# Optimization experiments

Measured on AMD Instinct MI355X. Metric: run time of the kernel, lower is better.

Reference implementation:

```python
import jax, jax.numpy as jnp
import numpy as np

HEADS = 16


def setup_inputs() -> dict:
    key = jax.random.key(0)
    k1, k2, k3, k4 = jax.random.split(key, 4)
    B, S, D = 2, 2048, 1024
    x = jax.random.normal(k1, (B, S, D), dtype=jnp.float32)
    scale = 0.02
    Wq = jax.random.normal(k2, (D, D), dtype=jnp.float32) * scale
    Wk = jax.random.normal(k3, (D, D), dtype=jnp.float32) * scale
    Wv = jax.random.normal(k4, (D, D), dtype=jnp.float32) * scale
    return {"x": x, "Wq": Wq, "Wk": Wk, "Wv": Wv}


def reference(x, Wq, Wk, Wv):
    B, S, D = x.shape
    H = HEADS
    dh = D // H
    # project and split heads: (B, S, D) -> (B, H, S, dh)
    def split_heads(t):
        return t.reshape(B, S, H, dh).transpose(0, 2, 1, 3)

    q = split_heads(x @ Wq)
    k = split_heads(x @ Wk)
    v = split_heads(x @ Wv)

    # scores: (B, H, S, S)
    scores = jnp.einsum("bhqd,bhkd->bhqk", q, k)
    causal_mask = jnp.triu(jnp.ones((S, S), dtype=bool), k=1)  # True above diagonal -> masked
    scores = jnp.where(causal_mask, -jnp.inf, scores) / jnp.sqrt(jnp.float32(dh))
    weights = jax.nn.softmax(scores, axis=-1)
    # dropout is identity at inference (eval mode)
    ctx = jnp.einsum("bhqk,bhkd->bhqd", weights, v)  # (B, H, S, dh)
    return ctx.transpose(0, 2, 1, 3).reshape(B, S, D)
```

## Files before the change

### kernel.cpp

```cpp
#include <hip/hip_runtime.h>
#include <hip/hip_bf16.h>
#include <cstdint>

#define BATCH  2
#define SEQ    2048
#define DMODEL 1024
#define NH     16
#define DH     64

typedef short bf16x8 __attribute__((ext_vector_type(8)));
typedef float f32x4  __attribute__((ext_vector_type(4)));
typedef unsigned short u16;

#define MFMA16(a, b, c) __builtin_amdgcn_mfma_f32_16x16x32_bf16((a), (b), (c), 0, 0, 0)

#define GLL(gp, lp) __builtin_amdgcn_global_load_lds( \
    (const __attribute__((address_space(1))) void*)(gp), \
    (__attribute__((address_space(3))) void*)(lp), 16, 0, 0)

#define SCL 0.18033688011112042f

#if __has_builtin(__builtin_amdgcn_exp2f)
#define EXP2(x) __builtin_amdgcn_exp2f(x)
#else
#define EXP2(x) __expf((x) * 0.69314718055994531f)
#endif

static __device__ __forceinline__ u16 f2bf(float f) {
  union { float f; unsigned int i; } u; u.f = f;
  unsigned int r = u.i + 0x7FFFu + ((u.i >> 16) & 1u);
  return (u16)(r >> 16);
}

__global__ __launch_bounds__(256) void convert_x_kernel(const float* __restrict__ X,
                                                        u16* __restrict__ Xb) {
  int idx = (blockIdx.x * 256 + threadIdx.x) * 8;
  float4 a = *reinterpret_cast<const float4*>(X + idx);
  float4 b = *reinterpret_cast<const float4*>(X + idx + 4);
  union { bf16x8 v; u16 u[8]; } pk;
  pk.u[0]=f2bf(a.x); pk.u[1]=f2bf(a.y); pk.u[2]=f2bf(a.z); pk.u[3]=f2bf(a.w);
  pk.u[4]=f2bf(b.x); pk.u[5]=f2bf(b.y); pk.u[6]=f2bf(b.z); pk.u[7]=f2bf(b.w);
  *reinterpret_cast<bf16x8*>(Xb + idx) = pk.v;
}

__global__ __launch_bounds__(256) void transpose_w_kernel(const float* __restrict__ W0,
                                                          const float* __restrict__ W1,
                                                          const float* __restrict__ W2,
                                                          u16* __restrict__ Wt) {
  const float* W = (blockIdx.z == 0) ? W0 : (blockIdx.z == 1) ? W1 : W2;
  const float sc = (blockIdx.z == 0) ? SCL : 1.0f;
  u16* out = Wt + (size_t)blockIdx.z * DMODEL * DMODEL;
  __shared__ float T[32][33];
  const int t = threadIdx.x;
  const int k0 = blockIdx.x * 32, n0 = blockIdx.y * 32;
  {
    int r = t >> 3, c = (t & 7) * 4;
    float4 v = *reinterpret_cast<const float4*>(W + (size_t)(k0 + r) * DMODEL + n0 + c);
    T[r][c] = v.x; T[r][c+1] = v.y; T[r][c+2] = v.z; T[r][c+3] = v.w;
  }
  __syncthreads();
  {
    int n = t >> 3, k = (t & 7) * 4;
    union { unsigned long long ll; u16 u[4]; } pk;
    pk.u[0] = f2bf(T[k][n] * sc);   pk.u[1] = f2bf(T[k+1][n] * sc);
    pk.u[2] = f2bf(T[k+2][n] * sc); pk.u[3] = f2bf(T[k+3][n] * sc);
    *reinterpret_cast<unsigned long long*>(out + (size_t)(n0 + n) * DMODEL + k0 + k) = pk.ll;
  }
}

__global__ __launch_bounds__(256) void qkv_mfma_kernel(const u16* __restrict__ Xb,
                                                       const u16* __restrict__ Wt,
                                                       u16* __restrict__ Y) {
  __shared__ u16 As[128 * 64];
  __shared__ u16 Bs[128 * 64];
  char* Ab = (char*)As; char* Bb = (char*)Bs;
  const int t = threadIdx.x;
  const int lane = t & 63;
  const int w = t >> 6;
  const int wr = w >> 1, wc = w & 1;
  const int l15 = lane & 15, lg = lane >> 4;
  const int row0 = blockIdx.x * 128;
  const int col0 = blockIdx.y * 128;
  const int z = blockIdx.z;
  const u16* Wz = Wt + (size_t)z * DMODEL * DMODEL;
  u16* Yz = Y + (size_t)z * ((size_t)BATCH * SEQ * DMODEL);

  f32x4 acc[4][4];
  #pragma unroll
  for (int mt = 0; mt < 4; ++mt)
    #pragma unroll
    for (int nt = 0; nt < 4; ++nt)
      acc[mt][nt] = (f32x4){0.f, 0.f, 0.f, 0.f};

  size_t aofs[4], bofs[4];
  #pragma unroll
  for (int it = 0; it < 4; ++it) {
    int row = it * 32 + (t >> 3);
    int sl  = (t & 7) ^ (row & 7);
    aofs[it] = (size_t)(row0 + row) * DMODEL + sl * 8;
    bofs[it] = (size_t)(col0 + row) * DMODEL + sl * 8;
  }

  for (int k0 = 0; k0 < DMODEL; k0 += 64) {
    __syncthreads();
    #pragma unroll
    for (int it = 0; it < 4; ++it) {
      GLL(Xb + aofs[it] + k0, Ab + it * 4096 + w * 1024);
      GLL(Wz + bofs[it] + k0, Bb + it * 4096 + w * 1024);
    }
    __syncthreads();
    #pragma unroll
    for (int c = 0; c < 2; ++c) {
      bf16x8 am[4], bn[4];
      int kof = c * 64 + lg * 16;
      #pragma unroll
      for (int mt = 0; mt < 4; ++mt) {
        int row = wr * 64 + mt * 16 + l15;
        am[mt] = *reinterpret_cast<const bf16x8*>(Ab + row * 128 + (kof ^ ((row & 7) << 4)));
      }
      #pragma unroll
      for (int nt = 0; nt < 4; ++nt) {
        int row = wc * 64 + nt * 16 + l15;
        bn[nt] = *reinterpret_cast<const bf16x8*>(Bb + row * 128 + (kof ^ ((row & 7) << 4)));
      }
      #pragma unroll
      for (int mt = 0; mt < 4; ++mt)
        #pragma unroll
        for (int nt = 0; nt < 4; ++nt)
          acc[mt][nt] = MFMA16(am[mt], bn[nt], acc[mt][nt]);
    }
  }

  #pragma unroll
  for (int mt = 0; mt < 4; ++mt) {
    #pragma unroll
    for (int i = 0; i < 4; ++i) {
      int bs = row0 + wr * 64 + mt * 16 + lg * 4 + i;
      int b = bs >> 11, s = bs & (SEQ - 1);
      #pragma unroll
      for (int nt = 0; nt < 4; ++nt) {
        int d = col0 + wc * 64 + nt * 16 + l15;
        int h = d >> 6, dd = d & (DH - 1);
        size_t off = (((size_t)b * NH + h) * SEQ + s) * DH + dd;
        Yz[off] = f2bf(acc[mt][nt][i]);
      }
    }
  }
}

__global__ __launch_bounds__(256) void transpose_v_kernel(const u16* __restrict__ V,
                                                          u16* __restrict__ Vt) {
  __shared__ u16 L[64][72];
  const int sb = blockIdx.x, h = blockIdx.y, b = blockIdx.z;
  const size_t hin  = ((size_t)b * NH + h) * (size_t)SEQ * DH;
  const size_t hout = ((size_t)b * NH + h) * (size_t)DH * SEQ;
  const int s0 = sb * 64;
  const int t = threadIdx.x;
  const int r = t >> 3, c = t & 7;
  #pragma unroll
  for (int it = 0; it < 2; ++it) {
    int row = r + it * 32;
    bf16x8 v = *reinterpret_cast<const bf16x8*>(V + hin + (size_t)(s0 + row) * DH + c * 8);
    *reinterpret_cast<bf16x8*>(&L[row][c * 8]) = v;
  }
  __syncthreads();
  #pragma unroll
  for (int it = 0; it < 2; ++it) {
    int d = r + it * 32;
    union { bf16x8 v; u16 u[8]; } pk;
    #pragma unroll
    for (int j = 0; j < 8; ++j) pk.u[j] = L[c * 8 + j][d];
    *reinterpret_cast<bf16x8*>(Vt + hout + (size_t)d * SEQ + s0 + c * 8) = pk.v;
  }
}

#define STAGE_KV(buf, kb)                                             \
  {                                                                   \
    const u16* kp_ = Kw + hq + (size_t)(kb) * (64 * DH);              \
    const u16* vp_ = Vt + hv + (size_t)(kb) * 64;                     \
    char* kd_ = (char*)(Ks[buf]) + dstb;                              \
    char* vd_ = (char*)(Vs[buf]) + dstb;                              \
    GLL(kp_ + kofs0, kd_);        GLL(vp_ + vofs0, vd_);              \
    GLL(kp_ + kofs1, kd_ + 1024); GLL(vp_ + vofs1, vd_ + 1024);       \
  }

#define TILE(kbv, curv, MASKED)                                                      \
  {                                                                                  \
    char* Kb = (char*)(Ks[curv]);                                                    \
    char* Vb = (char*)(Vs[curv]);                                                    \
    const int k0_ = (kbv) * 64;                                                      \
    __builtin_amdgcn_s_setprio(1);                                                   \
    _Pragma("unroll")                                                                \
    for (int kt = 0; kt < 4; ++kt) {                                                 \
      bf16x8 kf0 = *reinterpret_cast<const bf16x8*>(Kb + kvb0 + kt * 2048);          \
      bf16x8 kf1 = *reinterpret_cast<const bf16x8*>(Kb + kvb1 + kt * 2048);          \
      f32x4 sA = (f32x4){0.f, 0.f, 0.f, 0.f};                                        \
      f32x4 sB = (f32x4){0.f, 0.f, 0.f, 0.f};                                        \
      sA = MFMA16(kf0, qfA0, sA); sA = MFMA16(kf1, qfA1, sA);                        \
      sB = MFMA16(kf0, qfB0, sB); sB = MFMA16(kf1, qfB1, sB);                        \
      union { unsigned long long ll; __hip_bfloat16 bf[4]; } pA, pB;                 \
      _Pragma("unroll")                                                              \
      for (int i = 0; i < 4; ++i) {                                                  \
        float svA = sA[i], svB = sB[i];                                              \
        if (MASKED) {                                                                \
          int key = k0_ + kt * 16 + lg * 4 + i;                                      \
          if (key > qrowA) svA = -1e30f;                                             \
          if (key > qrowB) svB = -1e30f;                                             \
        }                                                                            \
        float eA = EXP2(svA), eB = EXP2(svB);                                        \
        l_A += eA; l_B += eB;                                                        \
        pA.bf[i] = __float2bfloat16(eA);                                             \
        pB.bf[i] = __float2bfloat16(eB);                                             \
      }                                                                              \
      int kx = (kt * 32) ^ xw;                                                       \
      *reinterpret_cast<unsigned long long*>(PbW + pwA + kx) = pA.ll;                \
      *reinterpret_cast<unsigned long long*>(PbW + pwB + kx) = pB.ll;                \
    }                                                                                \
    _Pragma("unroll")                                                                \
    for (int kc = 0; kc < 2; ++kc) {                                                 \
      const int tg = kc * 64;                                                        \
      bf16x8 paA = *reinterpret_cast<const bf16x8*>(PbW + (kvb0 ^ tg));              \
      bf16x8 paB = *reinterpret_cast<const bf16x8*>(PbW + (kvb0 ^ tg) + 2048);       \
      _Pragma("unroll")                                                              \
      for (int dt = 0; dt < 4; ++dt) {                                               \
        bf16x8 vv = *reinterpret_cast<const bf16x8*>(Vb + (kvb0 ^ tg) + dt * 2048);  \
        oA[dt] = MFMA16(paA, vv, oA[dt]);                                            \
        oB[dt] = MFMA16(paB, vv, oB[dt]);                                            \
      }                                                                              \
    }                                                                                \
    __builtin_amdgcn_s_setprio(0);                                                   \
  }

__global__ __launch_bounds__(256) void flash_mfma9_kernel(const u16* __restrict__ Qw,
                                                          const u16* __restrict__ Kw,
                                                          const u16* __restrict__ Vt,
                                                          float* __restrict__ Out) {
  __shared__ u16 Ks[2][64 * 64];
  __shared__ u16 Vs[2][64 * 64];
  __shared__ u16 Pl[4][32 * 64];

  const int wgid = blockIdx.x;
  const int qg = 15 - (wgid >> 5);
  const int g = wgid & 31;
  const int b = g >> 4, h = g & 15;
  const int nkv = 2 * qg + 2;

  const int t = threadIdx.x, lane = t & 63, w = t >> 6;
  const int l15 = lane & 15, lg = lane >> 4;
  char* PbW = (char*)Pl[w];
  const size_t hq = ((size_t)b * NH + h) * (size_t)SEQ * DH;
  const size_t hv = ((size_t)b * NH + h) * (size_t)DH * SEQ;

  int kofs0, kofs1, vofs0, vofs1;
  {
    int i0 = w * 128 + lane, i1 = i0 + 64;
    int r0 = i0 >> 3, r1 = i1 >> 3;
    kofs0 = r0 * DH  + (((i0 & 7) ^ (r0 & 7)) * 8);
    kofs1 = r1 * DH  + (((i1 & 7) ^ (r1 & 7)) * 8);
    vofs0 = r0 * SEQ + (((i0 & 7) ^ (r0 & 7)) * 8);
    vofs1 = r1 * SEQ + (((i1 & 7) ^ (r1 & 7)) * 8);
  }
  const int dstb = w * 2048;

  const int kvb0 = l15 * 128 + ((lg * 16) ^ ((l15 & 3) << 4)) + ((l15 & 4) << 4);
  const int kvb1 = kvb0 ^ 64;
  const int pwA  = l15 * 128 + ((lg * 8) ^ ((l15 & 1) << 4));
  const int pwB  = pwA + 2048;
  const int xw   = ((l15 >> 1) & 3) << 5;

  const int qbase = qg * 128 + w * 32;
  const int qrowA = qbase + l15;
  const int qrowB = qbase + 16 + l15;

  bf16x8 qfA0, qfA1, qfB0, qfB1;
  {
    const u16* qpA = Qw + hq + (size_t)qrowA * DH + lg * 8;
    const u16* qpB = Qw + hq + (size_t)qrowB * DH + lg * 8;
    qfA0 = *reinterpret_cast<const bf16x8*>(qpA);
    qfA1 = *reinterpret_cast<const bf16x8*>(qpA + 32);
    qfB0 = *reinterpret_cast<const bf16x8*>(qpB);
    qfB1 = *reinterpret_cast<const bf16x8*>(qpB + 32);
  }

  f32x4 oA[4], oB[4];
  #pragma unroll
  for (int dt = 0; dt < 4; ++dt) {
    oA[dt] = (f32x4){0.f, 0.f, 0.f, 0.f};
    oB[dt] = (f32x4){0.f, 0.f, 0.f, 0.f};
  }
  float l_A = 0.f, l_B = 0.f;

  STAGE_KV(0, 0);
  int cur = 0;
  int kb = 0;

  #pragma unroll 1
  for (; kb < nkv - 2; ++kb) {
    __syncthreads();
    STAGE_KV(cur ^ 1, kb + 1);
    TILE(kb, cur, 0);
    cur ^= 1;
  }
  __syncthreads();
  STAGE_KV(cur ^ 1, kb + 1);
  TILE(kb, cur, 1);
  cur ^= 1; ++kb;
  __syncthreads();
  TILE(kb, cur, 1);

  l_A += __shfl_xor(l_A, 16); l_A += __shfl_xor(l_A, 32);
  l_B += __shfl_xor(l_B, 16); l_B += __shfl_xor(l_B, 32);
  #pragma unroll
  for (int i = 0; i < 4; ++i) {
    float liA = __shfl(l_A, (lane & 48) + lg * 4 + i);
    float liB = __shfl(l_B, (lane & 48) + lg * 4 + i);
    float invA = 1.f / liA, invB = 1.f / liB;
    int qA = qbase + lg * 4 + i;
    int qB = qbase + 16 + lg * 4 + i;
    float* opA = Out + ((size_t)b * SEQ + qA) * DMODEL + h * DH + l15;
    float* opB = Out + ((size_t)b * SEQ + qB) * DMODEL + h * DH + l15;
    #pragma unroll
    for (int dt = 0; dt < 4; ++dt) {
      opA[dt * 16] = oA[dt][i] * invA;
      opB[dt * 16] = oB[dt][i] * invB;
    }
  }
}

extern "C" void kernel_launch(void* const* d_in, const int* in_sizes, int n_in,
                              void* d_out, int out_size, void* d_ws, size_t ws_size,
                              hipStream_t stream) {
  const float* x  = (const float*)d_in[0];
  const float* Wq = (const float*)d_in[1];
  const float* Wk = (const float*)d_in[2];
  const float* Wv = (const float*)d_in[3];
  float* out = (float*)d_out;

  u16* ws  = (u16*)d_ws;
  u16* qkv = ws;
  u16* xb  = ws + 12582912;
  u16* wt  = ws + 16777216;
  u16* vt  = ws + 19922944;

  convert_x_kernel<<<2048, 256, 0, stream>>>(x, xb);
  transpose_w_kernel<<<dim3(32, 32, 3), 256, 0, stream>>>(Wq, Wk, Wv, wt);
  qkv_mfma_kernel<<<dim3(32, 8, 3), 256, 0, stream>>>(xb, wt, qkv);
  transpose_v_kernel<<<dim3(32, NH, BATCH), 256, 0, stream>>>(qkv + 8388608, vt);
  flash_mfma9_kernel<<<512, 256, 0, stream>>>(qkv, qkv + 4194304, vt, out);
}
```

Before: 96.42 us.

## Split flash attention into single-wave blocks with per-wave KV staging

The flash attention kernel goes from 256-thread blocks, where four waves shared double-buffered K/V tiles, to 64-thread single-wave blocks that each handle 32 query rows. Each wave stages its own K/V tile, waits on vmcnt, and needs no block barriers. The grid grows to 2048 blocks in a snake ordering meant to balance causal work. This removes __syncthreads and the double buffering, but K/V loads are no longer overlapped with compute and each KV tile is fetched four times as often, which raises global/L2 traffic.

Result: slower. 99.11 us (+2.8%).

```diff
diff --git a/kernel.cpp b/kernel.cpp
--- a/kernel.cpp
+++ b/kernel.cpp
@@ -174,20 +174,25 @@
   }
 }
 
-#define STAGE_KV(buf, kb)                                             \
+#define STAGE(kb)                                                     \
   {                                                                   \
     const u16* kp_ = Kw + hq + (size_t)(kb) * (64 * DH);              \
     const u16* vp_ = Vt + hv + (size_t)(kb) * 64;                     \
-    char* kd_ = (char*)(Ks[buf]) + dstb;                              \
-    char* vd_ = (char*)(Vs[buf]) + dstb;                              \
-    GLL(kp_ + kofs0, kd_);        GLL(vp_ + vofs0, vd_);              \
-    GLL(kp_ + kofs1, kd_ + 1024); GLL(vp_ + vofs1, vd_ + 1024);       \
-  }
-
-#define TILE(kbv, curv, MASKED)                                                      \
+    _Pragma("unroll")                                                 \
+    for (int it = 0; it < 8; ++it) {                                  \
+      GLL(kp_ + kofs[it], (char*)Ksb + it * 1024);                    \
+      GLL(vp_ + vofs[it], (char*)Vsb + it * 1024);                    \
+    }                                                                 \
+  }
+
+#define WAITV()                                                       \
+  asm volatile("s_waitcnt vmcnt(0)" ::: "memory");                    \
+  __builtin_amdgcn_sched_barrier(0)
+
+#define TILE(kbv, MASKED)                                                            \
   {                                                                                  \
-    char* Kb = (char*)(Ks[curv]);                                                    \
-    char* Vb = (char*)(Vs[curv]);                                                    \
+    char* Kb = (char*)Ksb;                                                           \
+    char* Vb = (char*)Vsb;                                                           \
     const int k0_ = (kbv) * 64;                                                      \
     __builtin_amdgcn_s_setprio(1);                                                   \
     _Pragma("unroll")                                                                \
@@ -231,36 +236,36 @@
     __builtin_amdgcn_s_setprio(0);                                                   \
   }
 
-__global__ __launch_bounds__(256) void flash_mfma9_kernel(const u16* __restrict__ Qw,
+__global__ __launch_bounds__(64) void flash_mfma10_kernel(const u16* __restrict__ Qw,
                                                           const u16* __restrict__ Kw,
                                                           const u16* __restrict__ Vt,
                                                           float* __restrict__ Out) {
-  __shared__ u16 Ks[2][64 * 64];
-  __shared__ u16 Vs[2][64 * 64];
-  __shared__ u16 Pl[4][32 * 64];
+  __shared__ u16 Ksb[64 * 64];
+  __shared__ u16 Vsb[64 * 64];
+  __shared__ u16 Pw[32 * 64];
 
   const int wgid = blockIdx.x;
-  const int qg = 15 - (wgid >> 5);
   const int g = wgid & 31;
+  const int j = (wgid >> 5) & 7;
+  const int r = wgid >> 8;
+  const int qt = r * 8 + ((r & 1) ? (7 - j) : j);
   const int b = g >> 4, h = g & 15;
-  const int nkv = 2 * qg + 2;
-
-  const int t = threadIdx.x, lane = t & 63, w = t >> 6;
+  const int nkv = (qt >> 1) + 1;
+
+  const int lane = threadIdx.x;
   const int l15 = lane & 15, lg = lane >> 4;
-  char* PbW = (char*)Pl[w];
+  char* PbW = (char*)Pw;
   const size_t hq = ((size_t)b * NH + h) * (size_t)SEQ * DH;
   const size_t hv = ((size_t)b * NH + h) * (size_t)DH * SEQ;
 
-  int kofs0, kofs1, vofs0, vofs1;
-  {
-    int i0 = w * 128 + lane, i1 = i0 + 64;
-    int r0 = i0 >> 3, r1 = i1 >> 3;
-    kofs0 = r0 * DH  + (((i0 & 7) ^ (r0 & 7)) * 8);
-    kofs1 = r1 * DH  + (((i1 & 7) ^ (r1 & 7)) * 8);
-    vofs0 = r0 * SEQ + (((i0 & 7) ^ (r0 & 7)) * 8);
-    vofs1 = r1 * SEQ + (((i1 & 7) ^ (r1 & 7)) * 8);
-  }
-  const int dstb = w * 2048;
+  int kofs[8], vofs[8];
+  #pragma unroll
+  for (int it = 0; it < 8; ++it) {
+    int idx = it * 64 + lane;
+    int row = idx >> 3, sl = idx & 7;
+    kofs[it] = row * DH  + ((sl ^ (row & 7)) * 8);
+    vofs[it] = row * SEQ + ((sl ^ (row & 7)) * 8);
+  }
 
   const int kvb0 = l15 * 128 + ((lg * 16) ^ ((l15 & 3) << 4)) + ((l15 & 4) << 4);
   const int kvb1 = kvb0 ^ 64;
@@ -268,7 +273,7 @@
   const int pwB  = pwA + 2048;
   const int xw   = ((l15 >> 1) & 3) << 5;
 
-  const int qbase = qg * 128 + w * 32;
+  const int qbase = qt * 32;
   const int qrowA = qbase + l15;
   const int qrowB = qbase + 16 + l15;
 
@@ -290,23 +295,15 @@
   }
   float l_A = 0.f, l_B = 0.f;
 
-  STAGE_KV(0, 0);
-  int cur = 0;
-  int kb = 0;
-
   #pragma unroll 1
-  for (; kb < nkv - 2; ++kb) {
-    __syncthreads();
-    STAGE_KV(cur ^ 1, kb + 1);
-    TILE(kb, cur, 0);
-    cur ^= 1;
-  }
-  __syncthreads();
-  STAGE_KV(cur ^ 1, kb + 1);
-  TILE(kb, cur, 1);
-  cur ^= 1; ++kb;
-  __syncthreads();
-  TILE(kb, cur, 1);
+  for (int kb = 0; kb < nkv - 1; ++kb) {
+    STAGE(kb);
+    WAITV();
+    TILE(kb, 0);
+  }
+  STAGE(nkv - 1);
+  WAITV();
+  TILE(nkv - 1, 1);
 
   l_A += __shfl_xor(l_A, 16); l_A += __shfl_xor(l_A, 32);
   l_B += __shfl_xor(l_B, 16); l_B += __shfl_xor(l_B, 32);
@@ -346,5 +343,5 @@
   transpose_w_kernel<<<dim3(32, 32, 3), 256, 0, stream>>>(Wq, Wk, Wv, wt);
   qkv_mfma_kernel<<<dim3(32, 8, 3), 256, 0, stream>>>(xb, wt, qkv);
   transpose_v_kernel<<<dim3(32, NH, BATCH), 256, 0, stream>>>(qkv + 8388608, vt);
-  flash_mfma9_kernel<<<512, 256, 0, stream>>>(qkv, qkv + 4194304, vt, out);
-}
+  flash_mfma10_kernel<<<2048, 64, 0, stream>>>(qkv, qkv + 4194304, vt, out);
+}
```
